# Kernel optimization log

Hardware: AMD Instinct MI355X
Metric: run time of the kernel (lower is better)

Reference implementation:

```python
import jax, jax.numpy as jnp
from jax import lax
import numpy as np

EPS = 1e-5
ALPHA = 0.2  # LeakyReLU slope


def setup_inputs() -> dict:
    key = jax.random.key(0)
    ks = jax.random.split(key, 8)
    B, N, F_IN, HID, OUT, H = 32, 512, 256, 512, 512, 4
    D = OUT // H
    return {
        "x": jax.random.normal(ks[0], (B, N, F_IN), dtype=jnp.float32),
        "adj": jax.random.uniform(ks[1], (N, N), dtype=jnp.float32),
        "gc_w": jax.random.normal(ks[2], (F_IN, HID), dtype=jnp.float32) * 0.04,
        "gc_b": jax.random.normal(ks[3], (HID,), dtype=jnp.float32) * 0.04,
        "bn1_g": jnp.ones((HID,), jnp.float32),
        "bn1_b": jnp.zeros((HID,), jnp.float32),
        "bn1_m": jnp.zeros((HID,), jnp.float32),
        "bn1_v": jnp.ones((HID,), jnp.float32),
        "gat_w": jax.random.normal(ks[4], (H, D, HID), dtype=jnp.float32) * 0.04,
        "conv_w": jax.random.normal(ks[5], (OUT, OUT, 3), dtype=jnp.float32) * 0.02,
        "conv_b": jax.random.normal(ks[6], (OUT,), dtype=jnp.float32) * 0.02,
        "bn2_g": jnp.ones((OUT,), jnp.float32),
        "bn2_b": jnp.zeros((OUT,), jnp.float32),
        "bn2_m": jnp.zeros((OUT,), jnp.float32),
        "bn2_v": jnp.ones((OUT,), jnp.float32),
    }


def reference(x, adj, gc_w, gc_b, bn1_g, bn1_b, bn1_m, bn1_v, gat_w,
              conv_w, conv_b, bn2_g, bn2_b, bn2_m, bn2_v):
    # --- GraphConvolution: adj @ (x @ W) + b ---
    support = jnp.einsum('bnc,cd->bnd', x, gc_w)
    g = jnp.einsum('nm,bmd->bnd', adj, support) + gc_b  # [B,N,HID]
    # --- BatchNorm1d over channel dim (eval mode) + ReLU ---
    g = (g - bn1_m) * (bn1_g / jnp.sqrt(bn1_v + EPS)) + bn1_b
    g = jax.nn.relu(g)
    # --- Multi-head GAT (repeat/mul/sum == attention-weighted matmul) ---
    hh = jnp.einsum('bnf,hdf->bhnd', g, gat_w)           # per-head projections
    e = jnp.einsum('bhnd,bhmd->bhnm', hh, hh)            # logits [B,H,N,N]
    e = jnp.where(e > 0, e, ALPHA * e)                   # LeakyReLU
    att = jax.nn.softmax(e, axis=-1)
    o = jnp.einsum('bhnm,bhmd->bhnd', att, hh)
    B, H, N, D = o.shape
    o = o.transpose(0, 2, 1, 3).reshape(B, N, H * D)     # concat heads [B,N,OUT]
    # --- TCN block: conv1d(k=3,pad=1) over node axis + BN(eval) + ReLU ---
    xc = o.transpose(0, 2, 1)                            # [B,C,N]
    y = lax.conv_general_dilated(xc, conv_w, (1,), ((1, 1),),
                                 dimension_numbers=('NCH', 'OIH', 'NCH'))
    y = y + conv_b[None, :, None]
    y = (y - bn2_m[None, :, None]) * (bn2_g / jnp.sqrt(bn2_v + EPS))[None, :, None] + bn2_b[None, :, None]
    y = jax.nn.relu(y)
    return y.transpose(0, 2, 1)                          # [B,N,OUT]
```

## Files before the change

kernel.cpp:

```cpp
#include <hip/hip_runtime.h>
#include <math.h>

#define BATCH 32
#define NNODE 512
#define FIN   256
#define HIDC  512
#define OUTC  512
#define NHEAD 4
#define HDIM  128
#define EPSV  1e-5f
#define ALPHA_LR 0.2f

typedef _Float16 half8 __attribute__((ext_vector_type(8)));
typedef _Float16 half4v __attribute__((ext_vector_type(4)));
typedef float floatx4 __attribute__((ext_vector_type(4)));

#define GLOBAL_TO_LDS16(g, l)                                                  \
  __builtin_amdgcn_global_load_lds(                                            \
      (const __attribute__((address_space(1))) void*)(g),                      \
      (__attribute__((address_space(3))) void*)(l), 16, 0, 0)

__device__ __forceinline__ void split_gemm_acc(
    const _Float16* __restrict__ Ah, const _Float16* __restrict__ Al, int lda,
    const _Float16* __restrict__ Bh, const _Float16* __restrict__ Bl, int ldb,
    int K, int rowBase, int colBase,
    _Float16* sAh, _Float16* sAl, _Float16* sBh, _Float16* sBl,
    floatx4 acc[4][4], int tid) {
  const int lane = tid & 63, wave = tid >> 6;
  const int wr = (wave >> 1) * 64, wc = (wave & 1) * 64;
  const int fr = lane & 15, q = lane >> 4;
  const int r = tid >> 2, ko = (tid & 3) * 8;
  for (int k0 = 0; k0 < K; k0 += 32) {
    GLOBAL_TO_LDS16(&Ah[(size_t)(rowBase + r) * lda + k0 + ko], &sAh[tid * 8]);
    GLOBAL_TO_LDS16(&Ah[(size_t)(rowBase + r + 64) * lda + k0 + ko], &sAh[2048 + tid * 8]);
    GLOBAL_TO_LDS16(&Al[(size_t)(rowBase + r) * lda + k0 + ko], &sAl[tid * 8]);
    GLOBAL_TO_LDS16(&Al[(size_t)(rowBase + r + 64) * lda + k0 + ko], &sAl[2048 + tid * 8]);
    GLOBAL_TO_LDS16(&Bh[(size_t)(colBase + r) * ldb + k0 + ko], &sBh[tid * 8]);
    GLOBAL_TO_LDS16(&Bh[(size_t)(colBase + r + 64) * ldb + k0 + ko], &sBh[2048 + tid * 8]);
    GLOBAL_TO_LDS16(&Bl[(size_t)(colBase + r) * ldb + k0 + ko], &sBl[tid * 8]);
    GLOBAL_TO_LDS16(&Bl[(size_t)(colBase + r + 64) * ldb + k0 + ko], &sBl[2048 + tid * 8]);
    __syncthreads();
    half8 ah[4], al4[4], bh[4], bl4[4];
#pragma unroll
    for (int i = 0; i < 4; ++i) {
      ah[i]  = *(const half8*)&sAh[(wr + i * 16 + fr) * 32 + q * 8];
      al4[i] = *(const half8*)&sAl[(wr + i * 16 + fr) * 32 + q * 8];
    }
#pragma unroll
    for (int j = 0; j < 4; ++j) {
      bh[j]  = *(const half8*)&sBh[(wc + j * 16 + fr) * 32 + q * 8];
      bl4[j] = *(const half8*)&sBl[(wc + j * 16 + fr) * 32 + q * 8];
    }
#pragma unroll
    for (int i = 0; i < 4; ++i)
#pragma unroll
      for (int j = 0; j < 4; ++j) {
        acc[i][j] = __builtin_amdgcn_mfma_f32_16x16x32_f16(al4[i], bh[j], acc[i][j], 0, 0, 0);
        acc[i][j] = __builtin_amdgcn_mfma_f32_16x16x32_f16(ah[i], bl4[j], acc[i][j], 0, 0, 0);
        acc[i][j] = __builtin_amdgcn_mfma_f32_16x16x32_f16(ah[i], bh[j], acc[i][j], 0, 0, 0);
      }
    __syncthreads();
  }
}

__global__ __launch_bounds__(256) void k_prep(
    const float* __restrict__ adj, const float* __restrict__ gcw,
    const float* __restrict__ gatw, const float* __restrict__ cw,
    _Float16* __restrict__ ADJh, _Float16* __restrict__ ADJl,
    _Float16* __restrict__ GWh, _Float16* __restrict__ GWl,
    _Float16* __restrict__ GAh, _Float16* __restrict__ GAl,
    _Float16* __restrict__ WT, _Float16* __restrict__ OP) {
  const int i = blockIdx.x * 256 + threadIdx.x;
  if (i < 262144) {
    float v = adj[i];
    _Float16 h = (_Float16)v;
    ADJh[i] = h; ADJl[i] = (_Float16)(v - (float)h);
  } else if (i < 393216) {
    int j = i - 262144;
    int n = j >> 8, k = j & 255;
    float v = gcw[(size_t)k * HIDC + n];
    _Float16 h = (_Float16)v;
    GWh[j] = h; GWl[j] = (_Float16)(v - (float)h);
  } else if (i < 655360) {
    int j = i - 393216;
    float v = gatw[j];
    _Float16 h = (_Float16)v;
    GAh[j] = h; GAl[j] = (_Float16)(v - (float)h);
  } else if (i < 1441792) {
    int j = i - 655360;
    int n = j / 1536, kk = j - n * 1536;
    int tap = kk >> 9, ci = kk & 511;
    WT[j] = (_Float16)cw[(size_t)n * 1536 + ci * 3 + tap];
  } else if (i < 1474560) {
    int j = i - 1441792;
    int b = j >> 10, rs = (j >> 9) & 1, c = j & 511;
    OP[((size_t)b * 514 + rs * 513) * OUTC + c] = (_Float16)0.f;
  }
}

__global__ __launch_bounds__(256) void k_xsplit(const float* __restrict__ X,
                                                _Float16* __restrict__ Xh,
                                                _Float16* __restrict__ Xl) {
  const int i = (blockIdx.x * 256 + threadIdx.x) * 4;
  float4 v = *(const float4*)&X[i];
  half4v h, l;
  h[0] = (_Float16)v.x; l[0] = (_Float16)(v.x - (float)h[0]);
  h[1] = (_Float16)v.y; l[1] = (_Float16)(v.y - (float)h[1]);
  h[2] = (_Float16)v.z; l[2] = (_Float16)(v.z - (float)h[2]);
  h[3] = (_Float16)v.w; l[3] = (_Float16)(v.w - (float)h[3]);
  *(half4v*)&Xh[i] = h;
  *(half4v*)&Xl[i] = l;
}

__global__ __launch_bounds__(256) void k_support_t(
    const _Float16* __restrict__ GWh, const _Float16* __restrict__ GWl,
    const _Float16* __restrict__ Xh, const _Float16* __restrict__ Xl,
    _Float16* __restrict__ STh, _Float16* __restrict__ STl) {
  __shared__ _Float16 sm[4][4096];
  const int tid = threadIdx.x;
  const int rowBase = blockIdx.y * 128, colBase = blockIdx.x * 128;
  floatx4 acc[4][4] = {};
  split_gemm_acc(GWh, GWl, FIN, Xh, Xl, FIN, FIN, rowBase, colBase,
                 sm[0], sm[1], sm[2], sm[3], acc, tid);
  const int lane = tid & 63, wave = tid >> 6;
  const int wr = (wave >> 1) * 64, wc = (wave & 1) * 64;
  const int fr = lane & 15, q = lane >> 4;
#pragma unroll
  for (int i = 0; i < 4; ++i) {
    const int ch0 = rowBase + wr + i * 16 + q * 4;
#pragma unroll
    for (int rg = 0; rg < 4; ++rg) {
      size_t base = (size_t)(ch0 + rg) * 16384 + colBase + wc + fr;
#pragma unroll
      for (int j = 0; j < 4; ++j) {
        float v = acc[i][j][rg];
        _Float16 h = (_Float16)v;
        STh[base + j * 16] = h;
        STl[base + j * 16] = (_Float16)(v - (float)h);
      }
    }
  }
}

__global__ __launch_bounds__(256) void k_gcn(
    const _Float16* __restrict__ ADJh, const _Float16* __restrict__ ADJl,
    const _Float16* __restrict__ STh, const _Float16* __restrict__ STl,
    const float* __restrict__ gcb, const float* __restrict__ g1,
    const float* __restrict__ b1, const float* __restrict__ m1,
    const float* __restrict__ v1,
    _Float16* __restrict__ Gh, _Float16* __restrict__ Gl) {
  __shared__ _Float16 sm[4][4096];
  const int tid = threadIdx.x;
  const int rowBase = blockIdx.y * 128, colBase = blockIdx.x * 128;
  const int b = blockIdx.z;
  floatx4 acc[4][4] = {};
  split_gemm_acc(ADJh, ADJl, NNODE, STh + (size_t)b * NNODE, STl + (size_t)b * NNODE,
                 16384, NNODE, rowBase, colBase, sm[0], sm[1], sm[2], sm[3], acc, tid);
  const int lane = tid & 63, wave = tid >> 6;
  const int wr = (wave >> 1) * 64, wc = (wave & 1) * 64;
  const int fr = lane & 15, q = lane >> 4;
  float sc[4], of[4];
#pragma unroll
  for (int j = 0; j < 4; ++j) {
    int c = colBase + wc + j * 16 + fr;
    float s = g1[c] * rsqrtf(v1[c] + EPSV);
    sc[j] = s;
    of[j] = (gcb[c] - m1[c]) * s + b1[c];
  }
#pragma unroll
  for (int i = 0; i < 4; ++i) {
    const int n0 = rowBase + wr + i * 16 + q * 4;
#pragma unroll
    for (int rg = 0; rg < 4; ++rg) {
      size_t base = ((size_t)b * NNODE + n0 + rg) * HIDC + colBase + wc + fr;
#pragma unroll
      for (int j = 0; j < 4; ++j) {
        float v = fmaxf(fmaf(acc[i][j][rg], sc[j], of[j]), 0.0f);
        _Float16 h = (_Float16)v;
        Gh[base + j * 16] = h;
        Gl[base + j * 16] = (_Float16)(v - (float)h);
      }
    }
  }
}

__global__ __launch_bounds__(256) void k_hh(
    const _Float16* __restrict__ Gh, const _Float16* __restrict__ Gl,
    const _Float16* __restrict__ GAh, const _Float16* __restrict__ GAl,
    _Float16* __restrict__ HHh, _Float16* __restrict__ HHl) {
  __shared__ _Float16 sm[4][4096];
  const int tid = threadIdx.x;
  const int rowBase = blockIdx.y * 128, colBase = blockIdx.x * 128;
  floatx4 acc[4][4] = {};
  split_gemm_acc(Gh, Gl, HIDC, GAh, GAl, HIDC, HIDC, rowBase, colBase,
                 sm[0], sm[1], sm[2], sm[3], acc, tid);
  const int lane = tid & 63, wave = tid >> 6;
  const int wr = (wave >> 1) * 64, wc = (wave & 1) * 64;
  const int fr = lane & 15, q = lane >> 4;
#pragma unroll
  for (int i = 0; i < 4; ++i) {
    const int r0 = rowBase + wr + i * 16 + q * 4;
#pragma unroll
    for (int rg = 0; rg < 4; ++rg) {
      size_t base = (size_t)(r0 + rg) * OUTC + colBase + wc + fr;
#pragma unroll
      for (int j = 0; j < 4; ++j) {
        float v = acc[i][j][rg];
        _Float16 h = (_Float16)v;
        HHh[base + j * 16] = h;
        HHl[base + j * 16] = (_Float16)(v - (float)h);
      }
    }
  }
}

__global__ __launch_bounds__(256, 2) void k_attn(
    const _Float16* __restrict__ HHh, const _Float16* __restrict__ HHl,
    _Float16* __restrict__ OP) {
  __shared__ _Float16 sKh[128 * 32], sKl[128 * 32];
  __shared__ _Float16 sP[128 * 136];
  __shared__ _Float16 sVT[128 * 32];
  const int tid = threadIdx.x;
  const int lane = tid & 63, wave = tid >> 6;
  const int fr = lane & 15, q = lane >> 4;
  const int id = blockIdx.x;
  const int slot = id >> 3;
  const int g = (id & 7) + 8 * (slot >> 2);
  const int qBase = (slot & 3) * 128;
  const int bb = g >> 2, h = g & 3;
  const int w32 = wave * 32;
  const _Float16* Qh = HHh + ((size_t)bb * NNODE) * OUTC + h * HDIM;
  const _Float16* Ql = HHl + ((size_t)bb * NNODE) * OUTC + h * HDIM;
  const int r = tid >> 2, ko = (tid & 3) * 8;
  const int mB = tid >> 3, d0 = (tid & 7) * 16;

  half8 qh[2][4], ql[2][4];
#pragma unroll
  for (int i = 0; i < 2; ++i)
#pragma unroll
    for (int k0 = 0; k0 < 4; ++k0) {
      const size_t off = (size_t)(qBase + w32 + i * 16 + fr) * OUTC + k0 * 32 + q * 8;
      qh[i][k0] = *(const half8*)&Qh[off];
      ql[i][k0] = *(const half8*)&Ql[off];
    }

  floatx4 oacc[2][8] = {};
  float m_i[2][4], l_i[2][4];
#pragma unroll
  for (int i = 0; i < 2; ++i)
#pragma unroll
    for (int rg = 0; rg < 4; ++rg) { m_i[i][rg] = -1e30f; l_i[i][rg] = 0.f; }

  for (int kt = 0; kt < 4; ++kt) {
    floatx4 sacc[2][8] = {};
#pragma unroll
    for (int k0 = 0; k0 < 4; ++k0) {
      GLOBAL_TO_LDS16(&Qh[(size_t)(kt * 128 + r) * OUTC + k0 * 32 + ko], &sKh[tid * 8]);
      GLOBAL_TO_LDS16(&Qh[(size_t)(kt * 128 + r + 64) * OUTC + k0 * 32 + ko], &sKh[2048 + tid * 8]);
      GLOBAL_TO_LDS16(&Ql[(size_t)(kt * 128 + r) * OUTC + k0 * 32 + ko], &sKl[tid * 8]);
      GLOBAL_TO_LDS16(&Ql[(size_t)(kt * 128 + r + 64) * OUTC + k0 * 32 + ko], &sKl[2048 + tid * 8]);
      __syncthreads();
#pragma unroll
      for (int j = 0; j < 8; ++j) {
        half8 bh = *(const half8*)&sKh[(j * 16 + fr) * 32 + q * 8];
        half8 bl = *(const half8*)&sKl[(j * 16 + fr) * 32 + q * 8];
#pragma unroll
        for (int i = 0; i < 2; ++i) {
          sacc[i][j] = __builtin_amdgcn_mfma_f32_16x16x32_f16(ql[i][k0], bh, sacc[i][j], 0, 0, 0);
          sacc[i][j] = __builtin_amdgcn_mfma_f32_16x16x32_f16(qh[i][k0], bl, sacc[i][j], 0, 0, 0);
          sacc[i][j] = __builtin_amdgcn_mfma_f32_16x16x32_f16(qh[i][k0], bh, sacc[i][j], 0, 0, 0);
        }
      }
      __syncthreads();
    }
#pragma unroll
    for (int i = 0; i < 2; ++i)
#pragma unroll
      for (int j = 0; j < 8; ++j)
#pragma unroll
        for (int rg = 0; rg < 4; ++rg) {
          float v = sacc[i][j][rg];
          sacc[i][j][rg] = v > 0.f ? v : ALPHA_LR * v;
        }
#pragma unroll
    for (int i = 0; i < 2; ++i)
#pragma unroll
      for (int rg = 0; rg < 4; ++rg) {
        float mx = sacc[i][0][rg];
#pragma unroll
        for (int j = 1; j < 8; ++j) mx = fmaxf(mx, sacc[i][j][rg]);
        mx = fmaxf(mx, __shfl_xor(mx, 1));
        mx = fmaxf(mx, __shfl_xor(mx, 2));
        mx = fmaxf(mx, __shfl_xor(mx, 4));
        mx = fmaxf(mx, __shfl_xor(mx, 8));
        float mnew = fmaxf(m_i[i][rg], mx);
        float alpha = __expf(m_i[i][rg] - mnew);
        m_i[i][rg] = mnew;
        const int row = w32 + i * 16 + q * 4 + rg;
        float sum = 0.f;
#pragma unroll
        for (int j = 0; j < 8; ++j) {
          float p = __expf(sacc[i][j][rg] - mnew);
          sum += p;
          sP[row * 136 + j * 16 + fr] = (_Float16)p;
        }
        sum += __shfl_xor(sum, 1);
        sum += __shfl_xor(sum, 2);
        sum += __shfl_xor(sum, 4);
        sum += __shfl_xor(sum, 8);
        l_i[i][rg] = l_i[i][rg] * alpha + sum;
#pragma unroll
        for (int j = 0; j < 8; ++j) oacc[i][j][rg] *= alpha;
      }
    for (int ks = 0; ks < 4; ++ks) {
      __syncthreads();
      {
        const _Float16* src = &Qh[(size_t)(kt * 128 + ks * 32 + mB) * OUTC + d0];
        half8 v0 = *(const half8*)src;
        half8 v1 = *(const half8*)(src + 8);
#pragma unroll
        for (int e2 = 0; e2 < 8; ++e2) {
          sVT[(d0 + e2) * 32 + mB] = v0[e2];
          sVT[(d0 + 8 + e2) * 32 + mB] = v1[e2];
        }
      }
      __syncthreads();
      half8 pa[2];
#pragma unroll
      for (int i = 0; i < 2; ++i)
        pa[i] = *(const half8*)&sP[(w32 + i * 16 + fr) * 136 + ks * 32 + q * 8];
#pragma unroll
      for (int j = 0; j < 8; ++j) {
        half8 bv = *(const half8*)&sVT[(j * 16 + fr) * 32 + q * 8];
#pragma unroll
        for (int i = 0; i < 2; ++i)
          oacc[i][j] = __builtin_amdgcn_mfma_f32_16x16x32_f16(pa[i], bv, oacc[i][j], 0, 0, 0);
      }
    }
    __syncthreads();
  }
#pragma unroll
  for (int i = 0; i < 2; ++i)
#pragma unroll
    for (int rg = 0; rg < 4; ++rg) {
      const float inv = 1.0f / l_i[i][rg];
      const int node = qBase + w32 + i * 16 + q * 4 + rg;
      size_t base = ((size_t)bb * 514 + 1 + node) * OUTC + h * HDIM + fr;
#pragma unroll
      for (int j = 0; j < 8; ++j)
        OP[base + j * 16] = (_Float16)(oacc[i][j][rg] * inv);
    }
}

__global__ __launch_bounds__(256) void k_conv_mfma(
    const _Float16* __restrict__ OP, const _Float16* __restrict__ WT,
    const float* __restrict__ cb, const float* __restrict__ g2,
    const float* __restrict__ b2, const float* __restrict__ m2,
    const float* __restrict__ v2, float* __restrict__ Y) {
  __shared__ _Float16 At[128 * 32];
  __shared__ _Float16 Bt[128 * 32];
  const int tid = threadIdx.x;
  const int lane = tid & 63, wave = tid >> 6;
  const int wr = (wave >> 1) * 64, wc = (wave & 1) * 64;
  const int id = blockIdx.y * 4 + blockIdx.x;
  const int jj = id >> 3;
  const int rowBase = ((id & 7) * 16 + (jj >> 2)) * 128;
  const int colBase = (jj & 3) * 128;
  const int b = rowBase >> 9;
  const int n0 = rowBase & 511;
  const int r = tid >> 2;
  const int ko = (tid & 3) * 8;
  floatx4 acc[4][4] = {};
  for (int k0 = 0; k0 < 3 * OUTC; k0 += 32) {
    const int tap = k0 >> 9;
    const int cib = k0 & 511;
    const size_t abase = ((size_t)b * 514 + n0 + tap) * OUTC + cib + ko;
    GLOBAL_TO_LDS16(&OP[abase + (size_t)r * OUTC],        &At[tid * 8]);
    GLOBAL_TO_LDS16(&OP[abase + (size_t)(r + 64) * OUTC], &At[2048 + tid * 8]);
    GLOBAL_TO_LDS16(&WT[(size_t)(colBase + r) * 1536 + k0 + ko],      &Bt[tid * 8]);
    GLOBAL_TO_LDS16(&WT[(size_t)(colBase + r + 64) * 1536 + k0 + ko], &Bt[2048 + tid * 8]);
    __syncthreads();
    const int fr = lane & 15, q = lane >> 4;
    half8 af[4], bf[4];
#pragma unroll
    for (int i = 0; i < 4; ++i)
      af[i] = *(const half8*)&At[(wr + i * 16 + fr) * 32 + q * 8];
#pragma unroll
    for (int j = 0; j < 4; ++j)
      bf[j] = *(const half8*)&Bt[(wc + j * 16 + fr) * 32 + q * 8];
#pragma unroll
    for (int i = 0; i < 4; ++i)
#pragma unroll
      for (int j = 0; j < 4; ++j)
        acc[i][j] = __builtin_amdgcn_mfma_f32_16x16x32_f16(af[i], bf[j], acc[i][j], 0, 0, 0);
    __syncthreads();
  }
  const int fr = lane & 15, q = lane >> 4;
  float sc[4], of[4];
#pragma unroll
  for (int j = 0; j < 4; ++j) {
    int c = colBase + wc + j * 16 + fr;
    float s = g2[c] * rsqrtf(v2[c] + EPSV);
    sc[j] = s;
    of[j] = (cb[c] - m2[c]) * s + b2[c];
  }
#pragma unroll
  for (int i = 0; i < 4; ++i) {
    const int R0r = rowBase + wr + i * 16 + q * 4;
#pragma unroll
    for (int rg = 0; rg < 4; ++rg) {
      float* dst = &Y[(size_t)(R0r + rg) * OUTC + colBase + wc + fr];
#pragma unroll
      for (int j = 0; j < 4; ++j)
        dst[j * 16] = fmaxf(fmaf(acc[i][j][rg], sc[j], of[j]), 0.0f);
    }
  }
}

extern "C" void kernel_launch(void* const* d_in, const int* in_sizes, int n_in,
                              void* d_out, int out_size, void* d_ws, size_t ws_size,
                              hipStream_t stream) {
  const float* x     = (const float*)d_in[0];
  const float* adj   = (const float*)d_in[1];
  const float* gc_w  = (const float*)d_in[2];
  const float* gc_b  = (const float*)d_in[3];
  const float* bn1_g = (const float*)d_in[4];
  const float* bn1_b = (const float*)d_in[5];
  const float* bn1_m = (const float*)d_in[6];
  const float* bn1_v = (const float*)d_in[7];
  const float* gat_w = (const float*)d_in[8];
  const float* conv_w= (const float*)d_in[9];
  const float* conv_b= (const float*)d_in[10];
  const float* bn2_g = (const float*)d_in[11];
  const float* bn2_b = (const float*)d_in[12];
  const float* bn2_m = (const float*)d_in[13];
  const float* bn2_v = (const float*)d_in[14];
  float* out = (float*)d_out;

  char* ws = (char*)d_ws;
  _Float16* STh = (_Float16*)(ws + 0);
  _Float16* STl = (_Float16*)(ws + 16777216);
  _Float16* HHh = (_Float16*)(ws + 0);
  _Float16* HHl = (_Float16*)(ws + 16777216);
  _Float16* Xh  = (_Float16*)(ws + 33554432);
  _Float16* Xl  = (_Float16*)(ws + 41943040);
  _Float16* Gh  = (_Float16*)(ws + 33554432);
  _Float16* Gl  = (_Float16*)(ws + 50331648);
  _Float16* OP  = (_Float16*)(ws + 67108864);
  _Float16* WT  = (_Float16*)(ws + 83951616);
  _Float16* ADJh= (_Float16*)(ws + 85524480);
  _Float16* ADJl= (_Float16*)(ws + 86048768);
  _Float16* GWh = (_Float16*)(ws + 86573056);
  _Float16* GWl = (_Float16*)(ws + 86835200);
  _Float16* GAh = (_Float16*)(ws + 87097344);
  _Float16* GAl = (_Float16*)(ws + 87621632);

  k_prep<<<5760, 256, 0, stream>>>(adj, gc_w, gat_w, conv_w,
                                   ADJh, ADJl, GWh, GWl, GAh, GAl, WT, OP);
  k_xsplit<<<4096, 256, 0, stream>>>(x, Xh, Xl);
  k_support_t<<<dim3(128, 4), 256, 0, stream>>>(GWh, GWl, Xh, Xl, STh, STl);
  k_gcn<<<dim3(4, 4, 32), 256, 0, stream>>>(ADJh, ADJl, STh, STl, gc_b,
                                            bn1_g, bn1_b, bn1_m, bn1_v, Gh, Gl);
  k_hh<<<dim3(4, 128), 256, 0, stream>>>(Gh, Gl, GAh, GAl, HHh, HHl);
  k_attn<<<512, 256, 0, stream>>>(HHh, HHl, OP);
  k_conv_mfma<<<dim3(4, 128), 256, 0, stream>>>(OP, WT, conv_b,
                                                bn2_g, bn2_b, bn2_m, bn2_v, out);
}
```

Baseline: 296.7 us.

## Pre-transpose V in separate kernel and halve attention query tile

Adds a k_vt kernel that writes a transposed copy of the high half of HH per (batch, head) into workspace. The attention kernel can then load V^T directly into LDS with async global-to-LDS copies instead of scalar-scattering a transpose each step. The attention query tile drops from 128 to 64 rows per block, so the grid doubles to 1024 blocks and launch bounds target 3 blocks per CU. The per-step P staging buffer also shrinks, which cuts LDS use. In exchange there is an extra kernel launch plus a transpose round trip, and K is reloaded from global memory twice as often.

```diff
diff --git a/kernel.cpp b/kernel.cpp
--- a/kernel.cpp
+++ b/kernel.cpp
@@ -214,142 +214,147 @@
   }
 }
 
-__global__ __launch_bounds__(256, 2) void k_attn(
+__global__ __launch_bounds__(256) void k_vt(const _Float16* __restrict__ HHh,
+                                            _Float16* __restrict__ HHT) {
+  __shared__ _Float16 sT[128 * 132];
+  const int bt = blockIdx.x;
+  const int nt = bt & 3, g = bt >> 2;
+  const int bb = g >> 2, h = g & 3;
+  const int tid = threadIdx.x;
+  const int rr = tid >> 4, cc = (tid & 15) * 8;
+#pragma unroll
+  for (int it = 0; it < 8; ++it) {
+    int node = rr + it * 16;
+    half8 v = *(const half8*)&HHh[((size_t)bb * 512 + nt * 128 + node) * 512 + h * 128 + cc];
+#pragma unroll
+    for (int e = 0; e < 8; ++e) sT[(cc + e) * 132 + node] = v[e];
+  }
+  __syncthreads();
+#pragma unroll
+  for (int it = 0; it < 8; ++it) {
+    int d = rr + it * 16;
+    half8 v;
+#pragma unroll
+    for (int e = 0; e < 8; ++e) v[e] = sT[d * 132 + cc + e];
+    *(half8*)&HHT[((size_t)g * 128 + d) * 512 + nt * 128 + cc] = v;
+  }
+}
+
+__global__ __launch_bounds__(256, 3) void k_attn(
     const _Float16* __restrict__ HHh, const _Float16* __restrict__ HHl,
-    _Float16* __restrict__ OP) {
+    const _Float16* __restrict__ HHT, _Float16* __restrict__ OP) {
   __shared__ _Float16 sKh[128 * 32], sKl[128 * 32];
-  __shared__ _Float16 sP[128 * 136];
-  __shared__ _Float16 sVT[128 * 32];
+  __shared__ _Float16 sV[128 * 32];
+  __shared__ _Float16 sP[64 * 44];
   const int tid = threadIdx.x;
   const int lane = tid & 63, wave = tid >> 6;
   const int fr = lane & 15, q = lane >> 4;
   const int id = blockIdx.x;
   const int slot = id >> 3;
-  const int g = (id & 7) + 8 * (slot >> 2);
-  const int qBase = (slot & 3) * 128;
+  const int g = (id & 7) + 8 * (slot >> 3);
+  const int qBase = (slot & 7) * 64;
   const int bb = g >> 2, h = g & 3;
-  const int w32 = wave * 32;
-  const _Float16* Qh = HHh + ((size_t)bb * NNODE) * OUTC + h * HDIM;
-  const _Float16* Ql = HHl + ((size_t)bb * NNODE) * OUTC + h * HDIM;
+  const int w16 = wave * 16;
+  const _Float16* Qh = HHh + (size_t)bb * NNODE * OUTC + h * HDIM;
+  const _Float16* Ql = HHl + (size_t)bb * NNODE * OUTC + h * HDIM;
+  const _Float16* VT = HHT + (size_t)g * HDIM * NNODE;
   const int r = tid >> 2, ko = (tid & 3) * 8;
-  const int mB = tid >> 3, d0 = (tid & 7) * 16;
-
-  half8 qh[2][4], ql[2][4];
-#pragma unroll
-  for (int i = 0; i < 2; ++i)
+
+  half8 qh[4], ql[4];
+#pragma unroll
+  for (int k0 = 0; k0 < 4; ++k0) {
+    const size_t off = (size_t)(qBase + w16 + fr) * OUTC + k0 * 32 + q * 8;
+    qh[k0] = *(const half8*)&Qh[off];
+    ql[k0] = *(const half8*)&Ql[off];
+  }
+
+  floatx4 oacc[8] = {};
+  float m_i[4], l_i[4];
+#pragma unroll
+  for (int rg = 0; rg < 4; ++rg) { m_i[rg] = -1e30f; l_i[rg] = 0.f; }
+
+  for (int kt = 0; kt < 4; ++kt) {
+    const int ktb = kt * 128;
+    floatx4 sacc[8] = {};
 #pragma unroll
     for (int k0 = 0; k0 < 4; ++k0) {
-      const size_t off = (size_t)(qBase + w32 + i * 16 + fr) * OUTC + k0 * 32 + q * 8;
-      qh[i][k0] = *(const half8*)&Qh[off];
-      ql[i][k0] = *(const half8*)&Ql[off];
-    }
-
-  floatx4 oacc[2][8] = {};
-  float m_i[2][4], l_i[2][4];
-#pragma unroll
-  for (int i = 0; i < 2; ++i)
-#pragma unroll
-    for (int rg = 0; rg < 4; ++rg) { m_i[i][rg] = -1e30f; l_i[i][rg] = 0.f; }
-
-  for (int kt = 0; kt < 4; ++kt) {
-    floatx4 sacc[2][8] = {};
-#pragma unroll
-    for (int k0 = 0; k0 < 4; ++k0) {
-      GLOBAL_TO_LDS16(&Qh[(size_t)(kt * 128 + r) * OUTC + k0 * 32 + ko], &sKh[tid * 8]);
-      GLOBAL_TO_LDS16(&Qh[(size_t)(kt * 128 + r + 64) * OUTC + k0 * 32 + ko], &sKh[2048 + tid * 8]);
-      GLOBAL_TO_LDS16(&Ql[(size_t)(kt * 128 + r) * OUTC + k0 * 32 + ko], &sKl[tid * 8]);
-      GLOBAL_TO_LDS16(&Ql[(size_t)(kt * 128 + r + 64) * OUTC + k0 * 32 + ko], &sKl[2048 + tid * 8]);
+      GLOBAL_TO_LDS16(&Qh[(size_t)(ktb + r) * OUTC + k0 * 32 + ko], &sKh[tid * 8]);
+      GLOBAL_TO_LDS16(&Qh[(size_t)(ktb + r + 64) * OUTC + k0 * 32 + ko], &sKh[2048 + tid * 8]);
+      GLOBAL_TO_LDS16(&Ql[(size_t)(ktb + r) * OUTC + k0 * 32 + ko], &sKl[tid * 8]);
+      GLOBAL_TO_LDS16(&Ql[(size_t)(ktb + r + 64) * OUTC + k0 * 32 + ko], &sKl[2048 + tid * 8]);
       __syncthreads();
 #pragma unroll
       for (int j = 0; j < 8; ++j) {
         half8 bh = *(const half8*)&sKh[(j * 16 + fr) * 32 + q * 8];
         half8 bl = *(const half8*)&sKl[(j * 16 + fr) * 32 + q * 8];
-#pragma unroll
-        for (int i = 0; i < 2; ++i) {
-          sacc[i][j] = __builtin_amdgcn_mfma_f32_16x16x32_f16(ql[i][k0], bh, sacc[i][j], 0, 0, 0);
-          sacc[i][j] = __builtin_amdgcn_mfma_f32_16x16x32_f16(qh[i][k0], bl, sacc[i][j], 0, 0, 0);
-          sacc[i][j] = __builtin_amdgcn_mfma_f32_16x16x32_f16(qh[i][k0], bh, sacc[i][j], 0, 0, 0);
-        }
+        sacc[j] = __builtin_amdgcn_mfma_f32_16x16x32_f16(ql[k0], bh, sacc[j], 0, 0, 0);
+        sacc[j] = __builtin_amdgcn_mfma_f32_16x16x32_f16(qh[k0], bl, sacc[j], 0, 0, 0);
+        sacc[j] = __builtin_amdgcn_mfma_f32_16x16x32_f16(qh[k0], bh, sacc[j], 0, 0, 0);
       }
       __syncthreads();
     }
 #pragma unroll
-    for (int i = 0; i < 2; ++i)
-#pragma unroll
-      for (int j = 0; j < 8; ++j)
-#pragma unroll
-        for (int rg = 0; rg < 4; ++rg) {
-          float v = sacc[i][j][rg];
-          sacc[i][j][rg] = v > 0.f ? v : ALPHA_LR * v;
-        }
-#pragma unroll
-    for (int i = 0; i < 2; ++i)
+    for (int j = 0; j < 8; ++j)
 #pragma unroll
       for (int rg = 0; rg < 4; ++rg) {
-        float mx = sacc[i][0][rg];
-#pragma unroll
-        for (int j = 1; j < 8; ++j) mx = fmaxf(mx, sacc[i][j][rg]);
-        mx = fmaxf(mx, __shfl_xor(mx, 1));
-        mx = fmaxf(mx, __shfl_xor(mx, 2));
-        mx = fmaxf(mx, __shfl_xor(mx, 4));
-        mx = fmaxf(mx, __shfl_xor(mx, 8));
-        float mnew = fmaxf(m_i[i][rg], mx);
-        float alpha = __expf(m_i[i][rg] - mnew);
-        m_i[i][rg] = mnew;
-        const int row = w32 + i * 16 + q * 4 + rg;
-        float sum = 0.f;
-#pragma unroll
-        for (int j = 0; j < 8; ++j) {
-          float p = __expf(sacc[i][j][rg] - mnew);
-          sum += p;
-          sP[row * 136 + j * 16 + fr] = (_Float16)p;
-        }
-        sum += __shfl_xor(sum, 1);
-        sum += __shfl_xor(sum, 2);
-        sum += __shfl_xor(sum, 4);
-        sum += __shfl_xor(sum, 8);
-        l_i[i][rg] = l_i[i][rg] * alpha + sum;
-#pragma unroll
-        for (int j = 0; j < 8; ++j) oacc[i][j][rg] *= alpha;
-      }
+        float v = sacc[j][rg];
+        sacc[j][rg] = v > 0.f ? v : ALPHA_LR * v;
+      }
+#pragma unroll
+    for (int rg = 0; rg < 4; ++rg) {
+      float mx = sacc[0][rg];
+#pragma unroll
+      for (int j = 1; j < 8; ++j) mx = fmaxf(mx, sacc[j][rg]);
+      mx = fmaxf(mx, __shfl_xor(mx, 1));
+      mx = fmaxf(mx, __shfl_xor(mx, 2));
+      mx = fmaxf(mx, __shfl_xor(mx, 4));
+      mx = fmaxf(mx, __shfl_xor(mx, 8));
+      float mnew = fmaxf(m_i[rg], mx);
+      float alpha = __expf(m_i[rg] - mnew);
+      m_i[rg] = mnew;
+      float sum = 0.f;
+#pragma unroll
+      for (int j = 0; j < 8; ++j) {
+        float p = __expf(sacc[j][rg] - mnew);
+        sacc[j][rg] = p;
+        sum += p;
+      }
+      sum += __shfl_xor(sum, 1);
+      sum += __shfl_xor(sum, 2);
+      sum += __shfl_xor(sum, 4);
+      sum += __shfl_xor(sum, 8);
+      l_i[rg] = l_i[rg] * alpha + sum;
+#pragma unroll
+      for (int j = 0; j < 8; ++j) oacc[j][rg] *= alpha;
+    }
+#pragma unroll
     for (int ks = 0; ks < 4; ++ks) {
+#pragma unroll
+      for (int jj = 0; jj < 2; ++jj)
+#pragma unroll
+        for (int rg = 0; rg < 4; ++rg)
+          sP[(w16 + q * 4 + rg) * 44 + jj * 16 + fr] = (_Float16)sacc[2 * ks + jj][rg];
+      GLOBAL_TO_LDS16(&VT[(size_t)r * NNODE + ktb + ks * 32 + ko], &sV[tid * 8]);
+      GLOBAL_TO_LDS16(&VT[(size_t)(r + 64) * NNODE + ktb + ks * 32 + ko], &sV[2048 + tid * 8]);
       __syncthreads();
-      {
-        const _Float16* src = &Qh[(size_t)(kt * 128 + ks * 32 + mB) * OUTC + d0];
-        half8 v0 = *(const half8*)src;
-        half8 v1 = *(const half8*)(src + 8);
-#pragma unroll
-        for (int e2 = 0; e2 < 8; ++e2) {
-          sVT[(d0 + e2) * 32 + mB] = v0[e2];
-          sVT[(d0 + 8 + e2) * 32 + mB] = v1[e2];
-        }
+      half8 pa = *(const half8*)&sP[(w16 + fr) * 44 + q * 8];
+#pragma unroll
+      for (int j = 0; j < 8; ++j) {
+        half8 bv = *(const half8*)&sV[(j * 16 + fr) * 32 + q * 8];
+        oacc[j] = __builtin_amdgcn_mfma_f32_16x16x32_f16(pa, bv, oacc[j], 0, 0, 0);
       }
       __syncthreads();
-      half8 pa[2];
-#pragma unroll
-      for (int i = 0; i < 2; ++i)
-        pa[i] = *(const half8*)&sP[(w32 + i * 16 + fr) * 136 + ks * 32 + q * 8];
-#pragma unroll
-      for (int j = 0; j < 8; ++j) {
-        half8 bv = *(const half8*)&sVT[(j * 16 + fr) * 32 + q * 8];
-#pragma unroll
-        for (int i = 0; i < 2; ++i)
-          oacc[i][j] = __builtin_amdgcn_mfma_f32_16x16x32_f16(pa[i], bv, oacc[i][j], 0, 0, 0);
-      }
-    }
-    __syncthreads();
-  }
-#pragma unroll
-  for (int i = 0; i < 2; ++i)
-#pragma unroll
-    for (int rg = 0; rg < 4; ++rg) {
-      const float inv = 1.0f / l_i[i][rg];
-      const int node = qBase + w32 + i * 16 + q * 4 + rg;
-      size_t base = ((size_t)bb * 514 + 1 + node) * OUTC + h * HDIM + fr;
-#pragma unroll
-      for (int j = 0; j < 8; ++j)
-        OP[base + j * 16] = (_Float16)(oacc[i][j][rg] * inv);
-    }
+    }
+  }
+#pragma unroll
+  for (int rg = 0; rg < 4; ++rg) {
+    const float inv = 1.0f / l_i[rg];
+    const int node = qBase + w16 + q * 4 + rg;
+    size_t base = ((size_t)bb * 514 + 1 + node) * OUTC + h * HDIM + fr;
+#pragma unroll
+    for (int j = 0; j < 8; ++j)
+      OP[base + j * 16] = (_Float16)(oacc[j][rg] * inv);
+  }
 }
 
 __global__ __launch_bounds__(256) void k_conv_mfma(
@@ -446,6 +451,7 @@
   _Float16* Xl  = (_Float16*)(ws + 41943040);
   _Float16* Gh  = (_Float16*)(ws + 33554432);
   _Float16* Gl  = (_Float16*)(ws + 50331648);
+  _Float16* HHT = (_Float16*)(ws + 33554432);
   _Float16* OP  = (_Float16*)(ws + 67108864);
   _Float16* WT  = (_Float16*)(ws + 83951616);
   _Float16* ADJh= (_Float16*)(ws + 85524480);
@@ -462,7 +468,8 @@
   k_gcn<<<dim3(4, 4, 32), 256, 0, stream>>>(ADJh, ADJl, STh, STl, gc_b,
                                             bn1_g, bn1_b, bn1_m, bn1_v, Gh, Gl);
   k_hh<<<dim3(4, 128), 256, 0, stream>>>(Gh, Gl, GAh, GAl, HHh, HHl);
-  k_attn<<<512, 256, 0, stream>>>(HHh, HHl, OP);
+  k_vt<<<512, 256, 0, stream>>>(HHh, HHT);
+  k_attn<<<1024, 256, 0, stream>>>(HHh, HHl, HHT, OP);
   k_conv_mfma<<<dim3(4, 128), 256, 0, stream>>>(OP, WT, conv_b,
                                                 bn2_g, bn2_b, bn2_m, bn2_v, out);
 }
```

Measured after the change: 299.8 us. Within noise of the previous version (+1.0%).
